# Performance work log

Hardware: AMD Instinct MI355X
Metric: run time of the kernel (lower is better)

## Reference

```python
import jax, jax.numpy as jnp
import numpy as np

B, S, D = 4, 1024, 1024
NH, DH = 16, 64          # n_heads, head_dim (NH*DH == D)
FF = 4096                # hidden_dim
NE = 8                   # n_experts
OUT = 1024               # output_dim


def _scaled(k, shape, scale=0.02):
    return jax.random.normal(k, shape, jnp.float32) * scale


def setup_inputs() -> dict:
    ks = jax.random.split(jax.random.key(0), 12)
    return {
        "x": jax.random.normal(ks[0], (B, S, D), jnp.float32),
        "Wqkv": _scaled(ks[1], (D, 3 * D)),
        "Wo": _scaled(ks[2], (D, D)),
        "Wr": _scaled(ks[3], (D, D)),
        "u_bias": _scaled(ks[4], (NH, DH)),
        "v_bias": _scaled(ks[5], (NH, DH)),
        "ln1_g": jnp.ones((D,), jnp.float32), "ln1_b": jnp.zeros((D,), jnp.float32),
        "Wff1": _scaled(ks[6], (D, FF)), "bff1": jnp.zeros((FF,), jnp.float32),
        "Wff2": _scaled(ks[7], (FF, D)), "bff2": jnp.zeros((D,), jnp.float32),
        "ln2_g": jnp.ones((D,), jnp.float32), "ln2_b": jnp.zeros((D,), jnp.float32),
        "Wg": _scaled(ks[8], (D, NE)),
        "We1": _scaled(ks[9], (NE, D, FF)), "be1": jnp.zeros((NE, FF), jnp.float32),
        "We2": _scaled(ks[10], (NE, FF, D)), "be2": jnp.zeros((NE, D), jnp.float32),
        "ln3_g": jnp.ones((D,), jnp.float32), "ln3_b": jnp.zeros((D,), jnp.float32),
        "Wout": _scaled(ks[11], (D, OUT)),
    }


def _layer_norm(x, g, b):
    m = x.mean(-1, keepdims=True)
    v = x.var(-1, keepdims=True)
    return (x - m) * jax.lax.rsqrt(v + 1e-5) * g + b


def _rel_shift(x):
    # Transformer-XL relative shift. x: [B, H, Q, K] -> [B, H, Q, K]
    b, h, q, k = x.shape
    x = jnp.pad(x, ((0, 0), (0, 0), (0, 0), (1, 0)))  # [B,H,Q,K+1]
    return x.reshape(b, h, k + 1, q)[:, :, 1:, :].reshape(b, h, q, k)


def reference(x, Wqkv, Wo, Wr, u_bias, v_bias, ln1_g, ln1_b, Wff1, bff1,
              Wff2, bff2, ln2_g, ln2_b, Wg, We1, be1, We2, be2,
              ln3_g, ln3_b, Wout):
    b, s, d = x.shape
    # ---- TransformerXL attention stage (causal, relative positions) ----
    q, k, v = jnp.split(x @ Wqkv, 3, axis=-1)
    q = q.reshape(b, s, NH, DH)
    k = k.reshape(b, s, NH, DH)
    v = v.reshape(b, s, NH, DH)
    # sinusoidal relative position embedding, positions S-1 .. 0
    pos = jnp.arange(s - 1, -1, -1, dtype=jnp.float32)
    inv_freq = 1.0 / (10000.0 ** (jnp.arange(0, d, 2, dtype=jnp.float32) / d))
    sinusoid = pos[:, None] * inv_freq[None, :]
    pe = jnp.concatenate([jnp.sin(sinusoid), jnp.cos(sinusoid)], axis=-1)  # [S,D]
    r = (pe @ Wr).reshape(s, NH, DH)
    ac = jnp.einsum('bqhd,bkhd->bhqk', q + u_bias, k)
    bd = _rel_shift(jnp.einsum('bqhd,khd->bhqk', q + v_bias, r))
    scores = (ac + bd) * (1.0 / np.sqrt(DH).astype(np.float32))
    causal = jnp.tril(jnp.ones((s, s), bool))
    attn = jax.nn.softmax(jnp.where(causal, scores, -1e30), axis=-1)
    ctx = jnp.einsum('bhqk,bkhd->bqhd', attn, v).reshape(b, s, d)
    h = _layer_norm(x + ctx @ Wo, ln1_g, ln1_b)
    ff = jax.nn.relu(h @ Wff1 + bff1) @ Wff2 + bff2
    h = _layer_norm(h + ff, ln2_g, ln2_b)
    # ---- Switch Transformer MoE: top-1 routing, dispatch, combine ----
    probs = jax.nn.softmax(h @ Wg, axis=-1)           # [B,S,E]
    gate = probs.max(-1)                              # [B,S] top-1 gate value
    disp = jax.nn.one_hot(probs.argmax(-1), NE, dtype=h.dtype)  # [B,S,E]
    hid = jax.nn.relu(jnp.einsum('bsd,edf->besf', h, We1) + be1[None, :, None, :])
    eout = jnp.einsum('besf,efd->besd', hid, We2) + be2[None, :, None, :]
    moe = jnp.einsum('besd,bse->bsd', eout, disp) * gate[..., None]
    h = _layer_norm(h + moe, ln3_g, ln3_b)
    return h @ Wout
```

## Files before the change

### kernel.cpp

```cpp
#include <hip/hip_runtime.h>
#include <hip/hip_bf16.h>
#include <math.h>

static constexpr int Bx = 4, Sx = 1024, Dx = 1024, NHx = 16, DHx = 64;
static constexpr int FFx = 4096, NEx = 8, OUTx = 1024, BSx = Bx * Sx;

__device__ __forceinline__ void ld4f(const float* p, float* o) {
    float4 v = *(const float4*)p;
    o[0] = v.x; o[1] = v.y; o[2] = v.z; o[3] = v.w;
}

__global__ __launch_bounds__(256) void diag_k(float* __restrict__ out, int n, float val)
{
    int i = blockIdx.x * 256 + threadIdx.x;
    if (i < n) out[i] = val;
}

template<int RELU>
__global__ __launch_bounds__(256) void gemm_k(const float* __restrict__ A,
        const float* __restrict__ B, const float* __restrict__ bias,
        float* __restrict__ C, int M, int N, int K)
{
    __shared__ __align__(16) float As[16][64];
    __shared__ __align__(16) float Bs[16][64];
    const int tid = threadIdx.x;
    const int tx = tid & 15, ty = tid >> 4;
    const int m0 = blockIdx.y * 64, n0 = blockIdx.x * 64;
    float acc[4][4];
#pragma unroll
    for (int i = 0; i < 4; i++)
#pragma unroll
        for (int j = 0; j < 4; j++) acc[i][j] = 0.f;

    const int ma = tid >> 2, ka = (tid & 3) * 4;
    const int kb = tid >> 4, nb = (tid & 15) * 4;

    for (int k0 = 0; k0 < K; k0 += 16) {
        const float* ap = A + (size_t)(m0 + ma) * K + k0 + ka;
#pragma unroll
        for (int i = 0; i < 4; i++) As[ka + i][ma] = ap[i];
        const float* bp = B + (size_t)(k0 + kb) * N + n0 + nb;
#pragma unroll
        for (int i = 0; i < 4; i++) Bs[kb][nb + i] = bp[i];
        __syncthreads();
#pragma unroll
        for (int k = 0; k < 16; k++) {
            float a[4], bb[4];
            ld4f(&As[k][ty * 4], a);
            ld4f(&Bs[k][tx * 4], bb);
#pragma unroll
            for (int i = 0; i < 4; i++)
#pragma unroll
                for (int j = 0; j < 4; j++)
                    acc[i][j] = fmaf(a[i], bb[j], acc[i][j]);
        }
        __syncthreads();
    }
#pragma unroll
    for (int i = 0; i < 4; i++) {
        int m = m0 + ty * 4 + i;
#pragma unroll
        for (int j = 0; j < 4; j++) {
            int n = n0 + tx * 4 + j;
            float v = acc[i][j];
            if (bias) v += bias[n];
            if (RELU) v = fmaxf(v, 0.f);
            C[(size_t)m * N + n] = v;
        }
    }
}

__global__ __launch_bounds__(256) void pe_k(float* __restrict__ pe)
{
    int idx = blockIdx.x * 256 + threadIdx.x;
    int s = idx >> 9, j = idx & 511;
    double pos = (double)(Sx - 1 - s);
    double invf = exp(-((double)(2 * j) / (double)Dx) * log(10000.0));
    double ang = pos * invf;
    pe[(size_t)s * Dx + j]       = (float)sin(ang);
    pe[(size_t)s * Dx + 512 + j] = (float)cos(ang);
}

__global__ __launch_bounds__(256) void attn_k(const float* __restrict__ qkv,
        const float* __restrict__ r, const float* __restrict__ u_bias,
        const float* __restrict__ v_bias, float* __restrict__ ctx)
{
    const int qt = blockIdx.x;
    const int bh = blockIdx.y;
    const int b = bh >> 4, h = bh & 15;
    const int q0 = qt * 64;
    const int tid = threadIdx.x;
    const int tx = tid & 15, ty = tid >> 4;

    __shared__ __align__(16) float Qs[64][64];
    __shared__ __align__(16) float KP[2048];
    __shared__ __align__(16) float Vs[32][64];
    __shared__ __align__(16) float RBT[64][96];
    __shared__ float us[64], vs[64];

    for (int e = tid; e < 64 * 64; e += 256) {
        int qi = e >> 6, d = e & 63;
        Qs[d][qi] = qkv[((size_t)(b * Sx + q0 + qi)) * (3 * Dx) + h * DHx + d];
    }
    if (tid < 64) { us[tid] = u_bias[h * DHx + tid]; vs[tid] = v_bias[h * DHx + tid]; }

    float m_st[4], l_st[4], O[4][4];
#pragma unroll
    for (int i = 0; i < 4; i++) {
        m_st[i] = -1e30f; l_st[i] = 0.f;
#pragma unroll
        for (int j = 0; j < 4; j++) O[i][j] = 0.f;
    }

    const int nkt = 2 * qt + 2;
    for (int kt = 0; kt < nkt; kt++) {
        const int k0 = kt * 32;
        __syncthreads();
        for (int e = tid; e < 32 * 64; e += 256) {
            int ki = e >> 6, d = e & 63;
            size_t base = ((size_t)(b * Sx + k0 + ki)) * (3 * Dx) + h * DHx + d;
            KP[d * 32 + ki] = qkv[base + Dx];
            Vs[ki][d]       = qkv[base + 2 * Dx];
        }
        for (int e = tid; e < 64 * 96; e += 256) {
            int d = e / 96, t = e - 96 * d;
            int delta = q0 - k0 + t - 31;
            float val = 0.f;
            if (t < 95 && delta >= 0 && delta < Sx)
                val = r[(size_t)(Sx - 1 - delta) * Dx + h * DHx + d];
            RBT[d][t] = val;
        }
        __syncthreads();

        float sc[4][2];
#pragma unroll
        for (int i = 0; i < 4; i++) { sc[i][0] = 0.f; sc[i][1] = 0.f; }

        const int tb = 4 * ty - 2 * tx + 31;
#pragma unroll 4
        for (int d = 0; d < 64; d++) {
            float a[4];
            ld4f(&Qs[d][ty * 4], a);
            float k0v = KP[d * 32 + 2 * tx], k1v = KP[d * 32 + 2 * tx + 1];
            float uu = us[d], vv = vs[d];
            float rb[5];
#pragma unroll
            for (int t = 0; t < 5; t++) rb[t] = RBT[d][tb - 1 + t];
#pragma unroll
            for (int i = 0; i < 4; i++) {
                float qu = a[i] + uu, qv = a[i] + vv;
                sc[i][0] = fmaf(qu, k0v, fmaf(qv, rb[i + 1], sc[i][0]));
                sc[i][1] = fmaf(qu, k1v, fmaf(qv, rb[i],     sc[i][1]));
            }
        }

#pragma unroll
        for (int i = 0; i < 4; i++) {
            int qg = q0 + 4 * ty + i;
#pragma unroll
            for (int j = 0; j < 2; j++) {
                sc[i][j] *= 0.125f;
                if ((k0 + 2 * tx + j) > qg) sc[i][j] = -1e30f;
            }
            float mx = fmaxf(sc[i][0], sc[i][1]);
#pragma unroll
            for (int off = 8; off > 0; off >>= 1) mx = fmaxf(mx, __shfl_xor(mx, off, 16));
            float mnew = fmaxf(m_st[i], mx);
            float alpha = __expf(m_st[i] - mnew);
            m_st[i] = mnew;
            float rs = 0.f;
#pragma unroll
            for (int j = 0; j < 2; j++) { sc[i][j] = __expf(sc[i][j] - mnew); rs += sc[i][j]; }
#pragma unroll
            for (int off = 8; off > 0; off >>= 1) rs += __shfl_xor(rs, off, 16);
            l_st[i] = l_st[i] * alpha + rs;
#pragma unroll
            for (int j = 0; j < 4; j++) O[i][j] *= alpha;
        }

        __syncthreads();
#pragma unroll
        for (int i = 0; i < 4; i++)
#pragma unroll
            for (int j = 0; j < 2; j++)
                KP[(2 * tx + j) * 64 + 4 * ty + i] = sc[i][j];
        __syncthreads();
#pragma unroll 4
        for (int ki = 0; ki < 32; ki++) {
            float p[4], vv[4];
            ld4f(&KP[ki * 64 + ty * 4], p);
            ld4f(&Vs[ki][tx * 4], vv);
#pragma unroll
            for (int i = 0; i < 4; i++)
#pragma unroll
                for (int j = 0; j < 4; j++)
                    O[i][j] = fmaf(p[i], vv[j], O[i][j]);
        }
    }
#pragma unroll
    for (int i = 0; i < 4; i++) {
        float inv = (l_st[i] > 0.f) ? 1.f / l_st[i] : 0.f;
#pragma unroll
        for (int j = 0; j < 4; j++)
            ctx[((size_t)(b * Sx + q0 + ty * 4 + i)) * Dx + h * DHx + tx * 4 + j]
                = O[i][j] * inv;
    }
}

__global__ __launch_bounds__(256) void ln_k(const float* __restrict__ resid,
        const float* __restrict__ add, const float* __restrict__ g,
        const float* __restrict__ b, float* __restrict__ out)
{
    const int row = blockIdx.x, tid = threadIdx.x;
    const float* rr = resid + (size_t)row * Dx;
    const float* ar = add + (size_t)row * Dx;
    float v[4], s = 0.f, sq = 0.f;
#pragma unroll
    for (int i = 0; i < 4; i++) {
        int d = tid + i * 256;
        v[i] = rr[d] + ar[d];
        s += v[i]; sq += v[i] * v[i];
    }
#pragma unroll
    for (int off = 32; off > 0; off >>= 1) {
        s  += __shfl_down(s, off, 64);
        sq += __shfl_down(sq, off, 64);
    }
    __shared__ float red[8];
    int w = tid >> 6;
    if ((tid & 63) == 0) { red[w] = s; red[4 + w] = sq; }
    __syncthreads();
    s  = red[0] + red[1] + red[2] + red[3];
    sq = red[4] + red[5] + red[6] + red[7];
    float mean = s * (1.f / Dx);
    float var = fmaxf(sq * (1.f / Dx) - mean * mean, 0.f);
    float rstd = rsqrtf(var + 1e-5f);
#pragma unroll
    for (int i = 0; i < 4; i++) {
        int d = tid + i * 256;
        out[(size_t)row * Dx + d] = (v[i] - mean) * rstd * g[d] + b[d];
    }
}

__global__ __launch_bounds__(64) void route_k(const float* __restrict__ h,
        const float* __restrict__ Wg, float* __restrict__ gate,
        int* __restrict__ counts, int* __restrict__ lists)
{
    const int t = blockIdx.x, lane = threadIdx.x;
    float part[NEx];
#pragma unroll
    for (int e = 0; e < NEx; e++) part[e] = 0.f;
    const float* hr = h + (size_t)t * Dx;
    for (int d = lane; d < Dx; d += 64) {
        float hv = hr[d];
        const float* wr = Wg + (size_t)d * NEx;
#pragma unroll
        for (int e = 0; e < NEx; e++) part[e] = fmaf(hv, wr[e], part[e]);
    }
#pragma unroll
    for (int e = 0; e < NEx; e++)
#pragma unroll
        for (int off = 32; off > 0; off >>= 1)
            part[e] += __shfl_down(part[e], off, 64);
    if (lane == 0) {
        float mx = part[0]; int am = 0;
#pragma unroll
        for (int e = 1; e < NEx; e++) if (part[e] > mx) { mx = part[e]; am = e; }
        float ssum = 0.f;
#pragma unroll
        for (int e = 0; e < NEx; e++) ssum += expf(part[e] - mx);
        gate[t] = 1.f / ssum;
        int pos = atomicAdd(&counts[am], 1);
        lists[am * BSx + pos] = t;
    }
}

__global__ void zero_counts_k(int* counts) { if (threadIdx.x < NEx) counts[threadIdx.x] = 0; }

template<int PASS>
__global__ __launch_bounds__(256) void moe_gemm_k(const float* __restrict__ Act,
        const float* __restrict__ W, const float* __restrict__ bias,
        const int* __restrict__ lists, const int* __restrict__ counts,
        const float* __restrict__ gate, float* __restrict__ Out, int N, int K)
{
    const int e = blockIdx.z;
    const int cnt = counts[e];
    const int t0 = blockIdx.y * 64;
    if (t0 >= cnt) return;
    const int tid = threadIdx.x;
    const int tx = tid & 15, ty = tid >> 4;
    const int n0 = blockIdx.x * 64;

    __shared__ int toks[64];
    __shared__ __align__(16) float As[16][64];
    __shared__ __align__(16) float Bs[16][64];
    if (tid < 64) toks[tid] = (t0 + tid < cnt) ? lists[e * BSx + t0 + tid] : -1;
    __syncthreads();

    const float* We = W + (size_t)e * K * N;
    float acc[4][4];
#pragma unroll
    for (int i = 0; i < 4; i++)
#pragma unroll
        for (int j = 0; j < 4; j++) acc[i][j] = 0.f;

    const int ma = tid >> 2, ka = (tid & 3) * 4;
    const int kb = tid >> 4, nb = (tid & 15) * 4;

    for (int k0 = 0; k0 < K; k0 += 16) {
        int tok = toks[ma];
#pragma unroll
        for (int i = 0; i < 4; i++)
            As[ka + i][ma] = (tok >= 0) ? Act[(size_t)tok * K + k0 + ka + i] : 0.f;
        const float* bp = We + (size_t)(k0 + kb) * N + n0 + nb;
#pragma unroll
        for (int i = 0; i < 4; i++) Bs[kb][nb + i] = bp[i];
        __syncthreads();
#pragma unroll
        for (int k = 0; k < 16; k++) {
            float a[4], bb[4];
            ld4f(&As[k][ty * 4], a);
            ld4f(&Bs[k][tx * 4], bb);
#pragma unroll
            for (int i = 0; i < 4; i++)
#pragma unroll
                for (int j = 0; j < 4; j++)
                    acc[i][j] = fmaf(a[i], bb[j], acc[i][j]);
        }
        __syncthreads();
    }
#pragma unroll
    for (int i = 0; i < 4; i++) {
        int tok = toks[ty * 4 + i];
        if (tok < 0) continue;
#pragma unroll
        for (int j = 0; j < 4; j++) {
            int n = n0 + tx * 4 + j;
            float v = acc[i][j] + bias[(size_t)e * N + n];
            if (PASS == 1) Out[(size_t)tok * N + n] = fmaxf(v, 0.f);
            else           Out[(size_t)tok * N + n] = v * gate[tok];
        }
    }
}

extern "C" void kernel_launch(void* const* d_in, const int* in_sizes, int n_in,
                              void* d_out, int out_size, void* d_ws, size_t ws_size,
                              hipStream_t stream)
{
    (void)in_sizes; (void)n_in;
    const float* x      = (const float*)d_in[0];
    const float* Wqkv   = (const float*)d_in[1];
    const float* Wo     = (const float*)d_in[2];
    const float* Wr     = (const float*)d_in[3];
    const float* u_bias = (const float*)d_in[4];
    const float* v_bias = (const float*)d_in[5];
    const float* ln1_g  = (const float*)d_in[6];
    const float* ln1_b  = (const float*)d_in[7];
    const float* Wff1   = (const float*)d_in[8];
    const float* bff1   = (const float*)d_in[9];
    const float* Wff2   = (const float*)d_in[10];
    const float* bff2   = (const float*)d_in[11];
    const float* ln2_g  = (const float*)d_in[12];
    const float* ln2_b  = (const float*)d_in[13];
    const float* Wg     = (const float*)d_in[14];
    const float* We1    = (const float*)d_in[15];
    const float* be1    = (const float*)d_in[16];
    const float* We2    = (const float*)d_in[17];
    const float* be2    = (const float*)d_in[18];
    const float* ln3_g  = (const float*)d_in[19];
    const float* ln3_b  = (const float*)d_in[20];
    const float* Wout   = (const float*)d_in[21];
    float* out = (float*)d_out;

    char* base = (char*)d_ws;
    const size_t QKV_B = (size_t)BSx * 3 * Dx * 4;
    const size_t PE_B  = (size_t)Sx * Dx * 4;
    const size_t CTX_B = (size_t)BSx * Dx * 4;
    const size_t P2    = QKV_B + 2 * PE_B + CTX_B;
    const size_t NEEDED = P2 + 2 * CTX_B + 16384 + 256 + (size_t)NEx * BSx * 4;

    if (ws_size < NEEDED) {
        diag_k<<<(out_size + 255) / 256, 256, 0, stream>>>(out, out_size,
                                                           (float)(ws_size >> 20));
        return;
    }

    float* qkv  = (float*)(base);
    float* pe   = (float*)(base + QKV_B);
    float* rbuf = (float*)(base + QKV_B + PE_B);
    float* ctx  = (float*)(base + QKV_B + 2 * PE_B);
    float* ffh  = (float*)(base);
    float* tmp  = (float*)(base + P2);
    float* h    = (float*)(base + P2 + CTX_B);
    float* gate = (float*)(base + P2 + 2 * CTX_B);
    int* counts = (int*)(base + P2 + 2 * CTX_B + 16384);
    int* lists  = (int*)(base + P2 + 2 * CTX_B + 16384 + 256);

    gemm_k<0><<<dim3(3 * Dx / 64, BSx / 64), 256, 0, stream>>>(
        x, Wqkv, nullptr, qkv, BSx, 3 * Dx, Dx);
    pe_k<<<Sx * 512 / 256, 256, 0, stream>>>(pe);
    gemm_k<0><<<dim3(Dx / 64, Sx / 64), 256, 0, stream>>>(
        pe, Wr, nullptr, rbuf, Sx, Dx, Dx);
    attn_k<<<dim3(Sx / 64, Bx * NHx), 256, 0, stream>>>(qkv, rbuf, u_bias, v_bias, ctx);
    gemm_k<0><<<dim3(Dx / 64, BSx / 64), 256, 0, stream>>>(
        ctx, Wo, nullptr, tmp, BSx, Dx, Dx);
    ln_k<<<BSx, 256, 0, stream>>>(x, tmp, ln1_g, ln1_b, h);
    gemm_k<1><<<dim3(FFx / 64, BSx / 64), 256, 0, stream>>>(
        h, Wff1, bff1, ffh, BSx, FFx, Dx);
    gemm_k<0><<<dim3(Dx / 64, BSx / 64), 256, 0, stream>>>(
        ffh, Wff2, bff2, tmp, BSx, Dx, FFx);
    ln_k<<<BSx, 256, 0, stream>>>(h, tmp, ln2_g, ln2_b, h);
    zero_counts_k<<<1, 64, 0, stream>>>(counts);
    route_k<<<BSx, 64, 0, stream>>>(h, Wg, gate, counts, lists);
    moe_gemm_k<1><<<dim3(FFx / 64, BSx / 64, NEx), 256, 0, stream>>>(
        h, We1, be1, lists, counts, gate, ffh, FFx, Dx);
    moe_gemm_k<2><<<dim3(Dx / 64, BSx / 64, NEx), 256, 0, stream>>>(
        ffh, We2, be2, lists, counts, gate, tmp, Dx, FFx);
    ln_k<<<BSx, 256, 0, stream>>>(h, tmp, ln3_g, ln3_b, h);
    gemm_k<0><<<dim3(OUTx / 64, BSx / 64), 256, 0, stream>>>(
        h, Wout, nullptr, out, BSx, OUTx, Dx);
}
```

Measured before the change: 4.289 ms.

## Enlarge GEMM tiles to 128x128, balance causal attention blocks, swizzle LDS

Every dense and MoE GEMM now uses 128x128 tiles with an 8x8 register micro-tile per thread, vectorised float4 global loads and stores. This raises arithmetic intensity per shared-memory load and cuts global traffic. The attention kernel pairs query tile i with tile 15-i in each block so causal work is balanced across blocks, and it adds XOR-style index swizzles to the Q, K and P shared arrays to reduce bank conflicts. In exchange, register pressure rises (64 accumulators), which may lower occupancy, and the grids have fewer blocks.

```diff
diff --git a/kernel.cpp b/kernel.cpp
--- a/kernel.cpp
+++ b/kernel.cpp
@@ -21,51 +21,66 @@
         const float* __restrict__ B, const float* __restrict__ bias,
         float* __restrict__ C, int M, int N, int K)
 {
-    __shared__ __align__(16) float As[16][64];
-    __shared__ __align__(16) float Bs[16][64];
+    __shared__ __align__(16) float As[16][128];
+    __shared__ __align__(16) float Bs[16][128];
     const int tid = threadIdx.x;
     const int tx = tid & 15, ty = tid >> 4;
-    const int m0 = blockIdx.y * 64, n0 = blockIdx.x * 64;
-    float acc[4][4];
-#pragma unroll
-    for (int i = 0; i < 4; i++)
-#pragma unroll
-        for (int j = 0; j < 4; j++) acc[i][j] = 0.f;
+    const int m0 = blockIdx.y * 128, n0 = blockIdx.x * 128;
+    float acc[8][8];
+#pragma unroll
+    for (int i = 0; i < 8; i++)
+#pragma unroll
+        for (int j = 0; j < 8; j++) acc[i][j] = 0.f;
 
     const int ma = tid >> 2, ka = (tid & 3) * 4;
-    const int kb = tid >> 4, nb = (tid & 15) * 4;
+    const int kb = tid >> 4, nb = (tid & 15) * 8;
 
     for (int k0 = 0; k0 < K; k0 += 16) {
-        const float* ap = A + (size_t)(m0 + ma) * K + k0 + ka;
-#pragma unroll
-        for (int i = 0; i < 4; i++) As[ka + i][ma] = ap[i];
-        const float* bp = B + (size_t)(k0 + kb) * N + n0 + nb;
-#pragma unroll
-        for (int i = 0; i < 4; i++) Bs[kb][nb + i] = bp[i];
+        float a0[4], a1[4];
+        ld4f(A + (size_t)(m0 + ma) * K + k0 + ka, a0);
+        ld4f(A + (size_t)(m0 + ma + 64) * K + k0 + ka, a1);
+        float4 bv0 = *(const float4*)(B + (size_t)(k0 + kb) * N + n0 + nb);
+        float4 bv1 = *(const float4*)(B + (size_t)(k0 + kb) * N + n0 + nb + 4);
+#pragma unroll
+        for (int i = 0; i < 4; i++) {
+            As[ka + i][ma]      = a0[i];
+            As[ka + i][ma + 64] = a1[i];
+        }
+        *(float4*)&Bs[kb][nb]     = bv0;
+        *(float4*)&Bs[kb][nb + 4] = bv1;
         __syncthreads();
 #pragma unroll
         for (int k = 0; k < 16; k++) {
-            float a[4], bb[4];
-            ld4f(&As[k][ty * 4], a);
-            ld4f(&Bs[k][tx * 4], bb);
-#pragma unroll
-            for (int i = 0; i < 4; i++)
-#pragma unroll
-                for (int j = 0; j < 4; j++)
+            float a[8], bb[8];
+            ld4f(&As[k][4 * ty], a);
+            ld4f(&As[k][64 + 4 * ty], a + 4);
+            ld4f(&Bs[k][4 * tx], bb);
+            ld4f(&Bs[k][64 + 4 * tx], bb + 4);
+#pragma unroll
+            for (int i = 0; i < 8; i++)
+#pragma unroll
+                for (int j = 0; j < 8; j++)
                     acc[i][j] = fmaf(a[i], bb[j], acc[i][j]);
         }
         __syncthreads();
     }
 #pragma unroll
-    for (int i = 0; i < 4; i++) {
-        int m = m0 + ty * 4 + i;
-#pragma unroll
-        for (int j = 0; j < 4; j++) {
-            int n = n0 + tx * 4 + j;
-            float v = acc[i][j];
-            if (bias) v += bias[n];
-            if (RELU) v = fmaxf(v, 0.f);
-            C[(size_t)m * N + n] = v;
+    for (int ib = 0; ib < 2; ib++)
+#pragma unroll
+    for (int ii = 0; ii < 4; ii++) {
+        const int m = m0 + ib * 64 + 4 * ty + ii;
+#pragma unroll
+        for (int jb = 0; jb < 2; jb++) {
+            const int n = n0 + jb * 64 + 4 * tx;
+            float v[4];
+#pragma unroll
+            for (int jj = 0; jj < 4; jj++) {
+                float w = acc[ib * 4 + ii][jb * 4 + jj];
+                if (bias) w += bias[n + jj];
+                if (RELU) w = fmaxf(w, 0.f);
+                v[jj] = w;
+            }
+            *(float4*)&C[(size_t)m * N + n] = *(const float4*)v;
         }
     }
 }
@@ -85,125 +100,134 @@
         const float* __restrict__ r, const float* __restrict__ u_bias,
         const float* __restrict__ v_bias, float* __restrict__ ctx)
 {
-    const int qt = blockIdx.x;
     const int bh = blockIdx.y;
     const int b = bh >> 4, h = bh & 15;
-    const int q0 = qt * 64;
     const int tid = threadIdx.x;
     const int tx = tid & 15, ty = tid >> 4;
 
-    __shared__ __align__(16) float Qs[64][64];
+    __shared__ __align__(16) float Qs[64 * 64];
     __shared__ __align__(16) float KP[2048];
     __shared__ __align__(16) float Vs[32][64];
     __shared__ __align__(16) float RBT[64][96];
     __shared__ float us[64], vs[64];
 
-    for (int e = tid; e < 64 * 64; e += 256) {
-        int qi = e >> 6, d = e & 63;
-        Qs[d][qi] = qkv[((size_t)(b * Sx + q0 + qi)) * (3 * Dx) + h * DHx + d];
-    }
     if (tid < 64) { us[tid] = u_bias[h * DHx + tid]; vs[tid] = v_bias[h * DHx + tid]; }
 
-    float m_st[4], l_st[4], O[4][4];
-#pragma unroll
-    for (int i = 0; i < 4; i++) {
-        m_st[i] = -1e30f; l_st[i] = 0.f;
-#pragma unroll
-        for (int j = 0; j < 4; j++) O[i][j] = 0.f;
-    }
-
-    const int nkt = 2 * qt + 2;
-    for (int kt = 0; kt < nkt; kt++) {
-        const int k0 = kt * 32;
+    for (int half = 0; half < 2; half++) {
+        const int qt = half ? (15 - blockIdx.x) : blockIdx.x;
+        const int q0 = qt * 64;
+
         __syncthreads();
-        for (int e = tid; e < 32 * 64; e += 256) {
-            int ki = e >> 6, d = e & 63;
-            size_t base = ((size_t)(b * Sx + k0 + ki)) * (3 * Dx) + h * DHx + d;
-            KP[d * 32 + ki] = qkv[base + Dx];
-            Vs[ki][d]       = qkv[base + 2 * Dx];
-        }
-        for (int e = tid; e < 64 * 96; e += 256) {
-            int d = e / 96, t = e - 96 * d;
-            int delta = q0 - k0 + t - 31;
-            float val = 0.f;
-            if (t < 95 && delta >= 0 && delta < Sx)
-                val = r[(size_t)(Sx - 1 - delta) * Dx + h * DHx + d];
-            RBT[d][t] = val;
-        }
-        __syncthreads();
-
-        float sc[4][2];
-#pragma unroll
-        for (int i = 0; i < 4; i++) { sc[i][0] = 0.f; sc[i][1] = 0.f; }
-
-        const int tb = 4 * ty - 2 * tx + 31;
+        for (int e = tid; e < 64 * 64; e += 256) {
+            int qi = e >> 6, d = e & 63;
+            Qs[d * 64 + ((qi + 4 * d) & 63)] =
+                qkv[((size_t)(b * Sx + q0 + qi)) * (3 * Dx) + h * DHx + d];
+        }
+
+        float m_st[4], l_st[4], O[4][4];
+#pragma unroll
+        for (int i = 0; i < 4; i++) {
+            m_st[i] = -1e30f; l_st[i] = 0.f;
+#pragma unroll
+            for (int j = 0; j < 4; j++) O[i][j] = 0.f;
+        }
+
+        const int nkt = 2 * qt + 2;
+        for (int kt = 0; kt < nkt; kt++) {
+            const int k0 = kt * 32;
+            __syncthreads();
+            for (int e = tid; e < 32 * 64; e += 256) {
+                int ki = e >> 6, d = e & 63;
+                size_t base = ((size_t)(b * Sx + k0 + ki)) * (3 * Dx) + h * DHx + d;
+                KP[d * 32 + ((ki + d) & 31)] = qkv[base + Dx];
+                Vs[ki][d]                    = qkv[base + 2 * Dx];
+            }
+            for (int e = tid; e < 64 * 96; e += 256) {
+                int d = e / 96, t = e - 96 * d;
+                int delta = q0 - k0 + t - 31;
+                float val = 0.f;
+                if (t < 95 && delta >= 0 && delta < Sx)
+                    val = r[(size_t)(Sx - 1 - delta) * Dx + h * DHx + d];
+                RBT[d][t] = val;
+            }
+            __syncthreads();
+
+            float sc[4][2];
+#pragma unroll
+            for (int i = 0; i < 4; i++) { sc[i][0] = 0.f; sc[i][1] = 0.f; }
+
+            const int tb = 4 * ty - 2 * tx + 31;
 #pragma unroll 4
-        for (int d = 0; d < 64; d++) {
-            float a[4];
-            ld4f(&Qs[d][ty * 4], a);
-            float k0v = KP[d * 32 + 2 * tx], k1v = KP[d * 32 + 2 * tx + 1];
-            float uu = us[d], vv = vs[d];
-            float rb[5];
-#pragma unroll
-            for (int t = 0; t < 5; t++) rb[t] = RBT[d][tb - 1 + t];
+            for (int d = 0; d < 64; d++) {
+                float a[4];
+                ld4f(&Qs[d * 64 + ((4 * ty + 4 * d) & 63)], a);
+                float k0v = KP[d * 32 + ((2 * tx + d) & 31)];
+                float k1v = KP[d * 32 + ((2 * tx + 1 + d) & 31)];
+                float uu = us[d], vv = vs[d];
+                float rb[5];
+#pragma unroll
+                for (int t = 0; t < 5; t++) rb[t] = RBT[d][tb - 1 + t];
+#pragma unroll
+                for (int i = 0; i < 4; i++) {
+                    float qu = a[i] + uu, qv = a[i] + vv;
+                    sc[i][0] = fmaf(qu, k0v, fmaf(qv, rb[i + 1], sc[i][0]));
+                    sc[i][1] = fmaf(qu, k1v, fmaf(qv, rb[i],     sc[i][1]));
+                }
+            }
+
 #pragma unroll
             for (int i = 0; i < 4; i++) {
-                float qu = a[i] + uu, qv = a[i] + vv;
-                sc[i][0] = fmaf(qu, k0v, fmaf(qv, rb[i + 1], sc[i][0]));
-                sc[i][1] = fmaf(qu, k1v, fmaf(qv, rb[i],     sc[i][1]));
-            }
-        }
-
+                int qg = q0 + 4 * ty + i;
+#pragma unroll
+                for (int j = 0; j < 2; j++) {
+                    sc[i][j] *= 0.125f;
+                    if ((k0 + 2 * tx + j) > qg) sc[i][j] = -1e30f;
+                }
+                float mx = fmaxf(sc[i][0], sc[i][1]);
+#pragma unroll
+                for (int off = 8; off > 0; off >>= 1) mx = fmaxf(mx, __shfl_xor(mx, off, 16));
+                float mnew = fmaxf(m_st[i], mx);
+                float alpha = __expf(m_st[i] - mnew);
+                m_st[i] = mnew;
+                float rs = 0.f;
+#pragma unroll
+                for (int j = 0; j < 2; j++) { sc[i][j] = __expf(sc[i][j] - mnew); rs += sc[i][j]; }
+#pragma unroll
+                for (int off = 8; off > 0; off >>= 1) rs += __shfl_xor(rs, off, 16);
+                l_st[i] = l_st[i] * alpha + rs;
+#pragma unroll
+                for (int j = 0; j < 4; j++) O[i][j] *= alpha;
+            }
+
+            __syncthreads();
+#pragma unroll
+            for (int i = 0; i < 4; i++)
+#pragma unroll
+                for (int j = 0; j < 2; j++) {
+                    int kc = 2 * tx + j;
+                    KP[kc * 64 + ((4 * ty + i + 4 * kc) & 63)] = sc[i][j];
+                }
+            __syncthreads();
+#pragma unroll 4
+            for (int ki = 0; ki < 32; ki++) {
+                float p[4], vv[4];
+                ld4f(&KP[ki * 64 + ((4 * ty + 4 * ki) & 63)], p);
+                ld4f(&Vs[ki][tx * 4], vv);
+#pragma unroll
+                for (int i = 0; i < 4; i++)
+#pragma unroll
+                    for (int j = 0; j < 4; j++)
+                        O[i][j] = fmaf(p[i], vv[j], O[i][j]);
+            }
+        }
 #pragma unroll
         for (int i = 0; i < 4; i++) {
-            int qg = q0 + 4 * ty + i;
-#pragma unroll
-            for (int j = 0; j < 2; j++) {
-                sc[i][j] *= 0.125f;
-                if ((k0 + 2 * tx + j) > qg) sc[i][j] = -1e30f;
-            }
-            float mx = fmaxf(sc[i][0], sc[i][1]);
-#pragma unroll
-            for (int off = 8; off > 0; off >>= 1) mx = fmaxf(mx, __shfl_xor(mx, off, 16));
-            float mnew = fmaxf(m_st[i], mx);
-            float alpha = __expf(m_st[i] - mnew);
-            m_st[i] = mnew;
-            float rs = 0.f;
-#pragma unroll
-            for (int j = 0; j < 2; j++) { sc[i][j] = __expf(sc[i][j] - mnew); rs += sc[i][j]; }
-#pragma unroll
-            for (int off = 8; off > 0; off >>= 1) rs += __shfl_xor(rs, off, 16);
-            l_st[i] = l_st[i] * alpha + rs;
-#pragma unroll
-            for (int j = 0; j < 4; j++) O[i][j] *= alpha;
-        }
-
-        __syncthreads();
-#pragma unroll
-        for (int i = 0; i < 4; i++)
-#pragma unroll
-            for (int j = 0; j < 2; j++)
-                KP[(2 * tx + j) * 64 + 4 * ty + i] = sc[i][j];
-        __syncthreads();
-#pragma unroll 4
-        for (int ki = 0; ki < 32; ki++) {
-            float p[4], vv[4];
-            ld4f(&KP[ki * 64 + ty * 4], p);
-            ld4f(&Vs[ki][tx * 4], vv);
-#pragma unroll
-            for (int i = 0; i < 4; i++)
-#pragma unroll
-                for (int j = 0; j < 4; j++)
-                    O[i][j] = fmaf(p[i], vv[j], O[i][j]);
-        }
-    }
-#pragma unroll
-    for (int i = 0; i < 4; i++) {
-        float inv = (l_st[i] > 0.f) ? 1.f / l_st[i] : 0.f;
-#pragma unroll
-        for (int j = 0; j < 4; j++)
-            ctx[((size_t)(b * Sx + q0 + ty * 4 + i)) * Dx + h * DHx + tx * 4 + j]
-                = O[i][j] * inv;
+            float inv = (l_st[i] > 0.f) ? 1.f / l_st[i] : 0.f;
+#pragma unroll
+            for (int j = 0; j < 4; j++)
+                ctx[((size_t)(b * Sx + q0 + ty * 4 + i)) * Dx + h * DHx + tx * 4 + j]
+                    = O[i][j] * inv;
+        }
     }
 }
 
@@ -285,60 +309,77 @@
 {
     const int e = blockIdx.z;
     const int cnt = counts[e];
-    const int t0 = blockIdx.y * 64;
+    const int t0 = blockIdx.y * 128;
     if (t0 >= cnt) return;
     const int tid = threadIdx.x;
     const int tx = tid & 15, ty = tid >> 4;
-    const int n0 = blockIdx.x * 64;
-
-    __shared__ int toks[64];
-    __shared__ __align__(16) float As[16][64];
-    __shared__ __align__(16) float Bs[16][64];
-    if (tid < 64) toks[tid] = (t0 + tid < cnt) ? lists[e * BSx + t0 + tid] : -1;
+    const int n0 = blockIdx.x * 128;
+
+    __shared__ int toks[128];
+    __shared__ __align__(16) float As[16][128];
+    __shared__ __align__(16) float Bs[16][128];
+    if (tid < 128) toks[tid] = (t0 + tid < cnt) ? lists[e * BSx + t0 + tid] : -1;
     __syncthreads();
 
     const float* We = W + (size_t)e * K * N;
-    float acc[4][4];
-#pragma unroll
-    for (int i = 0; i < 4; i++)
-#pragma unroll
-        for (int j = 0; j < 4; j++) acc[i][j] = 0.f;
+    float acc[8][8];
+#pragma unroll
+    for (int i = 0; i < 8; i++)
+#pragma unroll
+        for (int j = 0; j < 8; j++) acc[i][j] = 0.f;
 
     const int ma = tid >> 2, ka = (tid & 3) * 4;
-    const int kb = tid >> 4, nb = (tid & 15) * 4;
+    const int kb = tid >> 4, nb = (tid & 15) * 8;
+    const int tokA = toks[ma], tokB = toks[ma + 64];
 
     for (int k0 = 0; k0 < K; k0 += 16) {
-        int tok = toks[ma];
-#pragma unroll
-        for (int i = 0; i < 4; i++)
-            As[ka + i][ma] = (tok >= 0) ? Act[(size_t)tok * K + k0 + ka + i] : 0.f;
-        const float* bp = We + (size_t)(k0 + kb) * N + n0 + nb;
-#pragma unroll
-        for (int i = 0; i < 4; i++) Bs[kb][nb + i] = bp[i];
+        float a0[4] = {0.f, 0.f, 0.f, 0.f}, a1[4] = {0.f, 0.f, 0.f, 0.f};
+        if (tokA >= 0) ld4f(Act + (size_t)tokA * K + k0 + ka, a0);
+        if (tokB >= 0) ld4f(Act + (size_t)tokB * K + k0 + ka, a1);
+        float4 bv0 = *(const float4*)(We + (size_t)(k0 + kb) * N + n0 + nb);
+        float4 bv1 = *(const float4*)(We + (size_t)(k0 + kb) * N + n0 + nb + 4);
+#pragma unroll
+        for (int i = 0; i < 4; i++) {
+            As[ka + i][ma]      = a0[i];
+            As[ka + i][ma + 64] = a1[i];
+        }
+        *(float4*)&Bs[kb][nb]     = bv0;
+        *(float4*)&Bs[kb][nb + 4] = bv1;
         __syncthreads();
 #pragma unroll
         for (int k = 0; k < 16; k++) {
-            float a[4], bb[4];
-            ld4f(&As[k][ty * 4], a);
-            ld4f(&Bs[k][tx * 4], bb);
-#pragma unroll
-            for (int i = 0; i < 4; i++)
-#pragma unroll
-                for (int j = 0; j < 4; j++)
+            float a[8], bb[8];
+            ld4f(&As[k][4 * ty], a);
+            ld4f(&As[k][64 + 4 * ty], a + 4);
+            ld4f(&Bs[k][4 * tx], bb);
+            ld4f(&Bs[k][64 + 4 * tx], bb + 4);
+#pragma unroll
+            for (int i = 0; i < 8; i++)
+#pragma unroll
+                for (int j = 0; j < 8; j++)
                     acc[i][j] = fmaf(a[i], bb[j], acc[i][j]);
         }
         __syncthreads();
     }
 #pragma unroll
-    for (int i = 0; i < 4; i++) {
-        int tok = toks[ty * 4 + i];
+    for (int ib = 0; ib < 2; ib++)
+#pragma unroll
+    for (int ii = 0; ii < 4; ii++) {
+        const int tok = toks[ib * 64 + 4 * ty + ii];
         if (tok < 0) continue;
-#pragma unroll
-        for (int j = 0; j < 4; j++) {
-            int n = n0 + tx * 4 + j;
-            float v = acc[i][j] + bias[(size_t)e * N + n];
-            if (PASS == 1) Out[(size_t)tok * N + n] = fmaxf(v, 0.f);
-            else           Out[(size_t)tok * N + n] = v * gate[tok];
+        const float gv = (PASS == 2) ? gate[tok] : 0.f;
+#pragma unroll
+        for (int jb = 0; jb < 2; jb++) {
+            const int n = n0 + jb * 64 + 4 * tx;
+            float v[4];
+#pragma unroll
+            for (int jj = 0; jj < 4; jj++) {
+                float w = acc[ib * 4 + ii][jb * 4 + jj] + bias[(size_t)e * N + n + jj];
+                if (PASS == 1) w = fmaxf(w, 0.f);
+                else           w = w * gv;
+                v[jj] = w;
+            }
+            *(float4*)&Out[(size_t)tok * N + n] = *(const float4*)v;
         }
     }
 }
@@ -396,27 +437,27 @@
     int* counts = (int*)(base + P2 + 2 * CTX_B + 16384);
     int* lists  = (int*)(base + P2 + 2 * CTX_B + 16384 + 256);
 
-    gemm_k<0><<<dim3(3 * Dx / 64, BSx / 64), 256, 0, stream>>>(
+    gemm_k<0><<<dim3(3 * Dx / 128, BSx / 128), 256, 0, stream>>>(
         x, Wqkv, nullptr, qkv, BSx, 3 * Dx, Dx);
     pe_k<<<Sx * 512 / 256, 256, 0, stream>>>(pe);
-    gemm_k<0><<<dim3(Dx / 64, Sx / 64), 256, 0, stream>>>(
+    gemm_k<0><<<dim3(Dx / 128, Sx / 128), 256, 0, stream>>>(
         pe, Wr, nullptr, rbuf, Sx, Dx, Dx);
-    attn_k<<<dim3(Sx / 64, Bx * NHx), 256, 0, stream>>>(qkv, rbuf, u_bias, v_bias, ctx);
-    gemm_k<0><<<dim3(Dx / 64, BSx / 64), 256, 0, stream>>>(
+    attn_k<<<dim3(8, Bx * NHx), 256, 0, stream>>>(qkv, rbuf, u_bias, v_bias, ctx);
+    gemm_k<0><<<dim3(Dx / 128, BSx / 128), 256, 0, stream>>>(
         ctx, Wo, nullptr, tmp, BSx, Dx, Dx);
     ln_k<<<BSx, 256, 0, stream>>>(x, tmp, ln1_g, ln1_b, h);
-    gemm_k<1><<<dim3(FFx / 64, BSx / 64), 256, 0, stream>>>(
+    gemm_k<1><<<dim3(FFx / 128, BSx / 128), 256, 0, stream>>>(
         h, Wff1, bff1, ffh, BSx, FFx, Dx);
-    gemm_k<0><<<dim3(Dx / 64, BSx / 64), 256, 0, stream>>>(
+    gemm_k<0><<<dim3(Dx / 128, BSx / 128), 256, 0, stream>>>(
         ffh, Wff2, bff2, tmp, BSx, Dx, FFx);
     ln_k<<<BSx, 256, 0, stream>>>(h, tmp, ln2_g, ln2_b, h);
     zero_counts_k<<<1, 64, 0, stream>>>(counts);
     route_k<<<BSx, 64, 0, stream>>>(h, Wg, gate, counts, lists);
-    moe_gemm_k<1><<<dim3(FFx / 64, BSx / 64, NEx), 256, 0, stream>>>(
+    moe_gemm_k<1><<<dim3(FFx / 128, BSx / 128, NEx), 256, 0, stream>>>(
         h, We1, be1, lists, counts, gate, ffh, FFx, Dx);
-    moe_gemm_k<2><<<dim3(Dx / 64, BSx / 64, NEx), 256, 0, stream>>>(
+    moe_gemm_k<2><<<dim3(Dx / 128, BSx / 128, NEx), 256, 0, stream>>>(
         ffh, We2, be2, lists, counts, gate, tmp, Dx, FFx);
     ln_k<<<BSx, 256, 0, stream>>>(h, tmp, ln3_g, ln3_b, h);
-    gemm_k<0><<<dim3(OUTx / 64, BSx / 64), 256, 0, stream>>>(
+    gemm_k<0><<<dim3(OUTx / 128, BSx / 128), 256, 0, stream>>>(
         h, Wout, nullptr, out, BSx, OUTx, Dx);
 }
```

Measured after the change: 4.441 ms. 3.5% more time.
